# Kernel tuning notes

Measured on AMD Instinct MI355X. Metric: run time of the kernel, lower is better.

Reference implementation:

```python
import jax, jax.numpy as jnp
import numpy as np

H, V, L = 1024, 50257, 512

def setup_inputs() -> dict:
    key = jax.random.key(0)
    ks = jax.random.split(key, 14)
    s = 0.02
    return {
        "input": jax.random.randint(ks[0], (1,), 0, V),
        "hidden": jax.random.normal(ks[1], (1, 1, H), jnp.float32),
        "encoder_outputs": jax.random.normal(ks[2], (L, H), jnp.float32),
        "emb": jax.random.normal(ks[3], (V, H), jnp.float32) * s,
        "attn_w": jax.random.normal(ks[4], (L, 2 * H), jnp.float32) * s,
        "attn_b": jnp.zeros((L,), jnp.float32),
        "comb_w": jax.random.normal(ks[5], (H, 2 * H), jnp.float32) * s,
        "comb_b": jnp.zeros((H,), jnp.float32),
        "w_ih": jax.random.normal(ks[6], (3 * H, H), jnp.float32) * s,
        "w_hh": jax.random.normal(ks[7], (3 * H, H), jnp.float32) * s,
        "b_ih": jnp.zeros((3 * H,), jnp.float32),
        "b_hh": jnp.zeros((3 * H,), jnp.float32),
        "out_w": jax.random.normal(ks[8], (V, H), jnp.float32) * s,
        "out_b": jnp.zeros((V,), jnp.float32),
    }

def reference(input, hidden, encoder_outputs, emb, attn_w, attn_b,
              comb_w, comb_b, w_ih, w_hh, b_ih, b_hh, out_w, out_b):
    # embedding lookup (dropout is identity in eval mode)
    e = emb[input]                       # (1, H)
    h0 = hidden[0]                       # (1, H)
    # attention over encoder outputs
    scores = jnp.concatenate([e, h0], axis=1) @ attn_w.T + attn_b   # (1, L)
    attn_weights = jax.nn.softmax(scores, axis=1)                    # (1, L)
    attn_applied = attn_weights @ encoder_outputs                    # (1, H)
    # combine + relu
    x = jnp.concatenate([e, attn_applied], axis=1) @ comb_w.T + comb_b
    x = jax.nn.relu(x)                   # (1, H)
    # single GRU step (PyTorch gate layout: r, z, n)
    gi = x @ w_ih.T + b_ih               # (1, 3H)
    gh = h0 @ w_hh.T + b_hh              # (1, 3H)
    i_r, i_z, i_n = jnp.split(gi, 3, axis=1)
    h_r, h_z, h_n = jnp.split(gh, 3, axis=1)
    r = jax.nn.sigmoid(i_r + h_r)
    z = jax.nn.sigmoid(i_z + h_z)
    n = jnp.tanh(i_n + r * h_n)
    h_new = (1.0 - z) * n + z * h0       # (1, H)
    # output projection + log_softmax
    logits = h_new @ out_w.T + out_b     # (1, V)
    out = jax.nn.log_softmax(logits, axis=1)
    return out, h_new[None], attn_weights
```

## Files before the change

### kernel.cpp

```cpp
#include <hip/hip_runtime.h>

#define H 1024
#define L 512
#define V 50257
#define LOGIT_BLOCKS 2048
#define ATTN_BLOCKS 128
#define COLS 8

__device__ __forceinline__ float dot4(float4 a, float4 b) {
    return a.x*b.x + a.y*b.y + a.z*b.z + a.w*b.w;
}

__device__ __forceinline__ float wave_reduce_sum(float v) {
    #pragma unroll
    for (int o = 32; o > 0; o >>= 1) v += __shfl_xor(v, o, 64);
    return v;
}

__global__ void k_pre(const float* __restrict__ emb, const int* __restrict__ input,
                      const float* __restrict__ hidden, const float* __restrict__ attn_w,
                      const float* __restrict__ attn_b, const float* __restrict__ w_hh,
                      const float* __restrict__ b_hh, const float* __restrict__ comb_w,
                      const float* __restrict__ comb_b,
                      float* __restrict__ scores, float* __restrict__ gh,
                      float* __restrict__ ce, float* __restrict__ xacc) {
    __shared__ float red[4];
    int task = blockIdx.x, t = threadIdx.x, lane = t & 63, wid = t >> 6;
    if (task == 4608) {
        ((float4*)xacc)[t] = make_float4(0.f, 0.f, 0.f, 0.f);
        return;
    }
    size_t erow = (size_t)input[0] * H;
    float acc;
    if (task < 512) {
        const float4* w = (const float4*)(attn_w + (size_t)task * (2 * H));
        acc = dot4(w[t], ((const float4*)(emb + erow))[t])
            + dot4(w[256 + t], ((const float4*)hidden)[t]);
    } else if (task < 3584) {
        int j = task - 512;
        acc = dot4(((const float4*)(w_hh + (size_t)j * H))[t], ((const float4*)hidden)[t]);
    } else {
        int h = task - 3584;
        acc = dot4(((const float4*)(comb_w + (size_t)h * (2 * H)))[t], ((const float4*)(emb + erow))[t]);
    }
    acc = wave_reduce_sum(acc);
    if (lane == 0) red[wid] = acc;
    __syncthreads();
    if (t == 0) {
        float s = red[0] + red[1] + red[2] + red[3];
        if (task < 512)       scores[task] = s + attn_b[task];
        else if (task < 3584) { int j = task - 512; gh[j] = s + b_hh[j]; }
        else                  { int h = task - 3584; ce[h] = s + comb_b[h]; }
    }
}

__global__ void k_attn_fused(const float* __restrict__ scores, const float* __restrict__ enc,
                             const float* __restrict__ comb_w,
                             float* __restrict__ attn_out, float* __restrict__ xacc) {
    __shared__ float w[512];
    __shared__ float red[4];
    __shared__ float s_acc[256];
    __shared__ float sM, sS;
    int t = threadIdx.x, lane = t & 63, wid = t >> 6, b = blockIdx.x;
    float s0 = scores[t], s1 = scores[t + 256];
    float m = fmaxf(s0, s1);
    #pragma unroll
    for (int o = 32; o > 0; o >>= 1) m = fmaxf(m, __shfl_xor(m, o, 64));
    if (lane == 0) red[wid] = m;
    __syncthreads();
    if (t == 0) sM = fmaxf(fmaxf(red[0], red[1]), fmaxf(red[2], red[3]));
    __syncthreads();
    float M = sM;
    float e0 = expf(s0 - M), e1 = expf(s1 - M);
    float ssum = wave_reduce_sum(e0 + e1);
    if (lane == 0) red[wid] = ssum;
    __syncthreads();
    if (t == 0) sS = red[0] + red[1] + red[2] + red[3];
    __syncthreads();
    float inv = 1.f / sS;
    w[t] = e0 * inv; w[t + 256] = e1 * inv;
    __syncthreads();
    if (b == 0) { attn_out[t] = w[t]; attn_out[t + 256] = w[t + 256]; }
    int col0 = b * COLS;
    int c  = t & 7;
    int rc = t >> 3;
    float acc = 0.f;
    #pragma unroll 4
    for (int l = rc; l < 512; l += 32) acc += w[l] * enc[(size_t)l * H + col0 + c];
    s_acc[t] = acc;
    __syncthreads();
    #pragma unroll
    for (int st = 128; st >= 8; st >>= 1) {
        if (t < st) s_acc[t] += s_acc[t + st];
        __syncthreads();
    }
    float4 aa0 = make_float4(s_acc[0], s_acc[1], s_acc[2], s_acc[3]);
    float4 aa1 = make_float4(s_acc[4], s_acc[5], s_acc[6], s_acc[7]);
    #pragma unroll
    for (int i = 0; i < 4; ++i) {
        int h = t + 256 * i;
        const float4* c2 = (const float4*)(comb_w + (size_t)h * (2 * H) + H + col0);
        float p = dot4(c2[0], aa0) + dot4(c2[1], aa1);
        atomicAdd(&xacc[h], p);
    }
}

__global__ void k_gru3(const float* __restrict__ w_ih, const float* __restrict__ b_ih,
                       const float* __restrict__ gh, const float* __restrict__ xacc,
                       const float* __restrict__ ce, const float* __restrict__ hidden,
                       float* __restrict__ hnew) {
    __shared__ float red[12];
    int h = blockIdx.x, t = threadIdx.x, lane = t & 63, wid = t >> 6;
    float4 xa = ((const float4*)xacc)[t];
    float4 cv = ((const float4*)ce)[t];
    float4 xv;
    xv.x = fmaxf(xa.x + cv.x, 0.f);
    xv.y = fmaxf(xa.y + cv.y, 0.f);
    xv.z = fmaxf(xa.z + cv.z, 0.f);
    xv.w = fmaxf(xa.w + cv.w, 0.f);
    float a0 = dot4(((const float4*)(w_ih + (size_t)h * H))[t], xv);
    float a1 = dot4(((const float4*)(w_ih + (size_t)(H + h) * H))[t], xv);
    float a2 = dot4(((const float4*)(w_ih + (size_t)(2 * H + h) * H))[t], xv);
    a0 = wave_reduce_sum(a0);
    a1 = wave_reduce_sum(a1);
    a2 = wave_reduce_sum(a2);
    if (lane == 0) { red[wid * 3] = a0; red[wid * 3 + 1] = a1; red[wid * 3 + 2] = a2; }
    __syncthreads();
    if (t == 0) {
        float g0 = 0.f, g1 = 0.f, g2 = 0.f;
        #pragma unroll
        for (int w2 = 0; w2 < 4; ++w2) {
            g0 += red[w2 * 3]; g1 += red[w2 * 3 + 1]; g2 += red[w2 * 3 + 2];
        }
        float r = 1.f / (1.f + expf(-(g0 + b_ih[h] + gh[h])));
        float z = 1.f / (1.f + expf(-(g1 + b_ih[H + h] + gh[H + h])));
        float n = tanhf(g2 + b_ih[2 * H + h] + r * gh[2 * H + h]);
        hnew[h] = (1.f - z) * n + z * hidden[h];
    }
}

__global__ void k_logits_lse(const float* __restrict__ out_w, const float* __restrict__ out_b,
                             const float* __restrict__ hvec, float* __restrict__ logits,
                             float* __restrict__ mpart, float* __restrict__ spart) {
    __shared__ float lm[4], ls[4];
    int lane = threadIdx.x & 63, wid = threadIdx.x >> 6;
    int gwave = blockIdx.x * 4 + wid;
    const int nwaves = LOGIT_BLOCKS * 4;
    float4 h4[4];
    #pragma unroll
    for (int j = 0; j < 4; ++j) h4[j] = ((const float4*)hvec)[j * 64 + lane];
    float m = -INFINITY, s = 0.f;
    for (int r = gwave; r < V; r += nwaves) {
        const float4* row = (const float4*)(out_w + (size_t)r * H);
        float acc = 0.f;
        #pragma unroll
        for (int j = 0; j < 4; ++j) acc += dot4(row[j * 64 + lane], h4[j]);
        acc = wave_reduce_sum(acc);
        float logit = acc + out_b[r];
        if (lane == 0) logits[r] = logit;
        if (logit > m) { s = s * expf(m - logit) + 1.f; m = logit; }
        else           { s += expf(logit - m); }
    }
    if (lane == 0) { lm[wid] = m; ls[wid] = s; }
    __syncthreads();
    if (threadIdx.x == 0) {
        float M = fmaxf(fmaxf(lm[0], lm[1]), fmaxf(lm[2], lm[3]));
        float S = 0.f;
        if (M > -INFINITY) {
            #pragma unroll
            for (int i = 0; i < 4; ++i) S += ls[i] * expf(lm[i] - M);
        }
        mpart[blockIdx.x] = M; spart[blockIdx.x] = S;
    }
}

__global__ void k_finalize(const float* __restrict__ mpart, const float* __restrict__ spart,
                           float* __restrict__ out) {
    __shared__ float lm[4], ls[4];
    __shared__ float sLogZ;
    int t = threadIdx.x, lane = t & 63, wid = t >> 6;
    float m = -INFINITY, s = 0.f;
    for (int i = t; i < LOGIT_BLOCKS; i += 256) {
        float m2 = mpart[i], s2 = spart[i];
        float mm = fmaxf(m, m2);
        if (mm > -INFINITY) s = s * expf(m - mm) + s2 * expf(m2 - mm);
        m = mm;
    }
    #pragma unroll
    for (int o = 32; o > 0; o >>= 1) {
        float m2 = __shfl_xor(m, o, 64), s2 = __shfl_xor(s, o, 64);
        float mm = fmaxf(m, m2);
        if (mm > -INFINITY) s = s * expf(m - mm) + s2 * expf(m2 - mm);
        m = mm;
    }
    if (lane == 0) { lm[wid] = m; ls[wid] = s; }
    __syncthreads();
    if (t == 0) {
        float M = fmaxf(fmaxf(lm[0], lm[1]), fmaxf(lm[2], lm[3]));
        float S = 0.f;
        #pragma unroll
        for (int i = 0; i < 4; ++i) S += ls[i] * expf(lm[i] - M);
        sLogZ = M + logf(S);
    }
    __syncthreads();
    int v = blockIdx.x * 256 + t;
    if (v < V) out[v] -= sLogZ;
}

extern "C" void kernel_launch(void* const* d_in, const int* in_sizes, int n_in,
                              void* d_out, int out_size, void* d_ws, size_t ws_size,
                              hipStream_t stream) {
    const int*   input  = (const int*)  d_in[0];
    const float* hidden = (const float*)d_in[1];
    const float* enc    = (const float*)d_in[2];
    const float* emb    = (const float*)d_in[3];
    const float* attn_w = (const float*)d_in[4];
    const float* attn_b = (const float*)d_in[5];
    const float* comb_w = (const float*)d_in[6];
    const float* comb_b = (const float*)d_in[7];
    const float* w_ih   = (const float*)d_in[8];
    const float* w_hh   = (const float*)d_in[9];
    const float* b_ih   = (const float*)d_in[10];
    const float* b_hh   = (const float*)d_in[11];
    const float* out_w  = (const float*)d_in[12];
    const float* out_b  = (const float*)d_in[13];

    float* out   = (float*)d_out;
    float* hnew  = out + V;
    float* attnw = out + V + H;

    float* ws     = (float*)d_ws;
    float* scores = ws;
    float* gh     = ws + 512;
    float* ce     = ws + 3584;
    float* xacc   = ws + 4608;
    float* mpart  = ws + 5632;
    float* spart  = ws + 7680;

    k_pre        <<<4609, 256, 0, stream>>>(emb, input, hidden, attn_w, attn_b,
                                            w_hh, b_hh, comb_w, comb_b, scores, gh, ce, xacc);
    k_attn_fused <<<ATTN_BLOCKS, 256, 0, stream>>>(scores, enc, comb_w, attnw, xacc);
    k_gru3       <<<1024, 256, 0, stream>>>(w_ih, b_ih, gh, xacc, ce, hidden, hnew);
    k_logits_lse <<<LOGIT_BLOCKS, 256, 0, stream>>>(out_w, out_b, hnew, out, mpart, spart);
    k_finalize   <<<(V + 255) / 256, 256, 0, stream>>>(mpart, spart, out);
}
```

Before: 63.19 us.

## Shrink scores kernel and overlap GRU/comb matvecs with attention blocks

```diff
diff --git a/kernel.cpp b/kernel.cpp
--- a/kernel.cpp
+++ b/kernel.cpp
@@ -4,8 +4,7 @@
 #define L 512
 #define V 50257
 #define LOGIT_BLOCKS 2048
-#define ATTN_BLOCKS 128
-#define COLS 8
+#define NATT 32
 
 __device__ __forceinline__ float dot4(float4 a, float4 b) {
     return a.x*b.x + a.y*b.y + a.z*b.z + a.w*b.w;
@@ -17,51 +16,64 @@
     return v;
 }
 
-__global__ void k_pre(const float* __restrict__ emb, const int* __restrict__ input,
-                      const float* __restrict__ hidden, const float* __restrict__ attn_w,
-                      const float* __restrict__ attn_b, const float* __restrict__ w_hh,
-                      const float* __restrict__ b_hh, const float* __restrict__ comb_w,
-                      const float* __restrict__ comb_b,
-                      float* __restrict__ scores, float* __restrict__ gh,
-                      float* __restrict__ ce, float* __restrict__ xacc) {
+__global__ void k_scores(const float* __restrict__ emb, const int* __restrict__ input,
+                         const float* __restrict__ hidden, const float* __restrict__ attn_w,
+                         const float* __restrict__ attn_b,
+                         float* __restrict__ scores, float* __restrict__ xacc) {
     __shared__ float red[4];
-    int task = blockIdx.x, t = threadIdx.x, lane = t & 63, wid = t >> 6;
-    if (task == 4608) {
+    int l = blockIdx.x, t = threadIdx.x;
+    if (l == 512) {
         ((float4*)xacc)[t] = make_float4(0.f, 0.f, 0.f, 0.f);
         return;
     }
     size_t erow = (size_t)input[0] * H;
-    float acc;
-    if (task < 512) {
-        const float4* w = (const float4*)(attn_w + (size_t)task * (2 * H));
-        acc = dot4(w[t], ((const float4*)(emb + erow))[t])
-            + dot4(w[256 + t], ((const float4*)hidden)[t]);
-    } else if (task < 3584) {
-        int j = task - 512;
-        acc = dot4(((const float4*)(w_hh + (size_t)j * H))[t], ((const float4*)hidden)[t]);
-    } else {
-        int h = task - 3584;
-        acc = dot4(((const float4*)(comb_w + (size_t)h * (2 * H)))[t], ((const float4*)(emb + erow))[t]);
-    }
+    const float4* w = (const float4*)(attn_w + (size_t)l * 2 * H);
+    float acc = dot4(w[t], ((const float4*)(emb + erow))[t])
+              + dot4(w[256 + t], ((const float4*)hidden)[t]);
     acc = wave_reduce_sum(acc);
-    if (lane == 0) red[wid] = acc;
-    __syncthreads();
-    if (t == 0) {
-        float s = red[0] + red[1] + red[2] + red[3];
-        if (task < 512)       scores[task] = s + attn_b[task];
-        else if (task < 3584) { int j = task - 512; gh[j] = s + b_hh[j]; }
-        else                  { int h = task - 3584; ce[h] = s + comb_b[h]; }
-    }
-}
-
-__global__ void k_attn_fused(const float* __restrict__ scores, const float* __restrict__ enc,
-                             const float* __restrict__ comb_w,
-                             float* __restrict__ attn_out, float* __restrict__ xacc) {
-    __shared__ float w[512];
+    if ((t & 63) == 0) red[t >> 6] = acc;
+    __syncthreads();
+    if (t == 0) scores[l] = red[0] + red[1] + red[2] + red[3] + attn_b[l];
+}
+
+__global__ void k_mid(const float* __restrict__ scores, const float* __restrict__ enc,
+                      const float* __restrict__ comb_w, const float* __restrict__ comb_b,
+                      const float* __restrict__ hidden, const float* __restrict__ w_hh,
+                      const float* __restrict__ b_hh, const float* __restrict__ emb,
+                      const int* __restrict__ input,
+                      float* __restrict__ attnw, float* __restrict__ xacc,
+                      float* __restrict__ gh, float* __restrict__ ce) {
     __shared__ float red[4];
+    int bid = blockIdx.x, t = threadIdx.x, lane = t & 63, wid = t >> 6;
+
+    if (bid >= NATT) {
+        float acc;
+        int task = bid - NATT;
+        if (task < 3072) {
+            acc = dot4(((const float4*)(w_hh + (size_t)task * H))[t],
+                       ((const float4*)hidden)[t]);
+        } else {
+            int h = task - 3072;
+            size_t erow = (size_t)input[0] * H;
+            acc = dot4(((const float4*)(comb_w + (size_t)h * (2 * H)))[t],
+                       ((const float4*)(emb + erow))[t]);
+        }
+        acc = wave_reduce_sum(acc);
+        if (lane == 0) red[wid] = acc;
+        __syncthreads();
+        if (t == 0) {
+            float s = red[0] + red[1] + red[2] + red[3];
+            if (task < 3072) gh[task] = s + b_hh[task];
+            else             { int h = task - 3072; ce[h] = s + comb_b[h]; }
+        }
+        return;
+    }
+
+    __shared__ float s_w[512];
     __shared__ float s_acc[256];
     __shared__ float sM, sS;
-    int t = threadIdx.x, lane = t & 63, wid = t >> 6, b = blockIdx.x;
+    int c0 = bid * 32;
+
     float s0 = scores[t], s1 = scores[t + 256];
     float m = fmaxf(s0, s1);
     #pragma unroll
@@ -78,30 +90,35 @@
     if (t == 0) sS = red[0] + red[1] + red[2] + red[3];
     __syncthreads();
     float inv = 1.f / sS;
-    w[t] = e0 * inv; w[t + 256] = e1 * inv;
-    __syncthreads();
-    if (b == 0) { attn_out[t] = w[t]; attn_out[t + 256] = w[t + 256]; }
-    int col0 = b * COLS;
-    int c  = t & 7;
-    int rc = t >> 3;
-    float acc = 0.f;
-    #pragma unroll 4
-    for (int l = rc; l < 512; l += 32) acc += w[l] * enc[(size_t)l * H + col0 + c];
-    s_acc[t] = acc;
-    __syncthreads();
-    #pragma unroll
-    for (int st = 128; st >= 8; st >>= 1) {
-        if (t < st) s_acc[t] += s_acc[t + st];
+    s_w[t] = e0 * inv; s_w[t + 256] = e1 * inv;
+    __syncthreads();
+    if (bid == 0) { attnw[t] = s_w[t]; attnw[t + 256] = s_w[t + 256]; }
+
+    {
+        int c = t & 31, rc = t >> 5;
+        float a = 0.f;
+        #pragma unroll 8
+        for (int l = rc; l < 512; l += 8) a += s_w[l] * enc[(size_t)l * H + c0 + c];
+        s_acc[t] = a;
         __syncthreads();
-    }
-    float4 aa0 = make_float4(s_acc[0], s_acc[1], s_acc[2], s_acc[3]);
-    float4 aa1 = make_float4(s_acc[4], s_acc[5], s_acc[6], s_acc[7]);
-    #pragma unroll
-    for (int i = 0; i < 4; ++i) {
-        int h = t + 256 * i;
-        const float4* c2 = (const float4*)(comb_w + (size_t)h * (2 * H) + H + col0);
-        float p = dot4(c2[0], aa0) + dot4(c2[1], aa1);
-        atomicAdd(&xacc[h], p);
+        #pragma unroll
+        for (int st = 128; st >= 32; st >>= 1) {
+            if (t < st) s_acc[t] += s_acc[t + st];
+            __syncthreads();
+        }
+    }
+
+    {
+        int lane32 = t & 31;
+        int hw     = t >> 5;
+        float aav  = s_acc[lane32];
+        #pragma unroll 4
+        for (int hrow = hw; hrow < H; hrow += 8) {
+            float v = comb_w[(size_t)hrow * (2 * H) + H + c0 + lane32] * aav;
+            #pragma unroll
+            for (int o = 16; o > 0; o >>= 1) v += __shfl_xor(v, o, 64);
+            if (lane32 == 0) atomicAdd(&xacc[hrow], v);
+        }
     }
 }
 
@@ -237,9 +254,11 @@
     float* mpart  = ws + 5632;
     float* spart  = ws + 7680;
 
-    k_pre        <<<4609, 256, 0, stream>>>(emb, input, hidden, attn_w, attn_b,
-                                            w_hh, b_hh, comb_w, comb_b, scores, gh, ce, xacc);
-    k_attn_fused <<<ATTN_BLOCKS, 256, 0, stream>>>(scores, enc, comb_w, attnw, xacc);
+    k_scores     <<<513, 256, 0, stream>>>(emb, input, hidden, attn_w, attn_b,
+                                           scores, xacc);
+    k_mid        <<<NATT + 3072 + 1024, 256, 0, stream>>>(scores, enc, comb_w, comb_b,
+                                                          hidden, w_hh, b_hh, emb, input,
+                                                          attnw, xacc, gh, ce);
     k_gru3       <<<1024, 256, 0, stream>>>(w_ih, b_ih, gh, xacc, ce, hidden, hnew);
     k_logits_lse <<<LOGIT_BLOCKS, 256, 0, stream>>>(out_w, out_b, hnew, out, mpart, spart);
     k_finalize   <<<(V + 255) / 256, 256, 0, stream>>>(mpart, spart, out);
```

New measurement: 133.9 us. 2.12x slower.
